# Kernel tuning notes

Hardware: AMD Instinct MI355X
Metric: run time of the kernel (lower is better)

The kernel has to match this reference:

```python
import jax, jax.numpy as jnp
import numpy as np

N, M, F0, FB, F, H, NC, NCONV = 60000, 12, 92, 41, 64, 128, 2000, 3
EPS = 1e-5


def setup_inputs() -> dict:
    key = jax.random.key(0)
    ks = jax.random.split(key, 12)
    s = 0.05
    return {
        "atom_fea": jax.random.normal(ks[0], (N, F0), jnp.float32),
        "nbr_fea": jax.random.normal(ks[1], (N, M, FB), jnp.float32),
        "nbr_fea_idx": jax.random.randint(ks[2], (N, M), 0, N),
        "crystal_atom_idx": jnp.sort(jax.random.randint(ks[3], (N,), 0, NC)),
        "W_emb": jax.random.normal(ks[4], (F0, F), jnp.float32) * s,
        "b_emb": jnp.zeros((F,), jnp.float32),
        "W_full": jax.random.normal(ks[5], (NCONV, 2 * F + FB, 2 * F), jnp.float32) * s,
        "b_full": jnp.zeros((NCONV, 2 * F), jnp.float32),
        "g1": jnp.ones((NCONV, 2 * F), jnp.float32),
        "be1": jnp.zeros((NCONV, 2 * F), jnp.float32),
        "g2": jnp.ones((NCONV, F), jnp.float32),
        "be2": jnp.zeros((NCONV, F), jnp.float32),
        "W_fc": jax.random.normal(ks[6], (F, H), jnp.float32) * s,
        "b_fc": jnp.zeros((H,), jnp.float32),
        "W_out": jax.random.normal(ks[7], (H, 1), jnp.float32) * s,
        "b_out": jnp.zeros((1,), jnp.float32),
    }


def _bn(x, g, b):
    # training-mode batch norm over leading (row) dim
    m = x.mean(axis=0)
    v = x.var(axis=0)
    return (x - m) * jax.lax.rsqrt(v + EPS) * g + b


def _conv_layer(x, nbr_fea, nbr_fea_idx, Wf, bf, g1, be1, g2, be2):
    n, m = nbr_fea_idx.shape
    f = x.shape[1]
    atom_nbr = x[nbr_fea_idx]  # (N, M, F) gather
    total = jnp.concatenate(
        [jnp.broadcast_to(x[:, None, :], (n, m, f)), atom_nbr, nbr_fea], axis=2
    )  # (N, M, 2F+FB)
    gated = total @ Wf + bf  # (N, M, 2F)
    gated = _bn(gated.reshape(-1, 2 * f), g1, be1).reshape(n, m, 2 * f)
    nbr_filter, nbr_core = jnp.split(gated, 2, axis=2)
    summed = jnp.sum(jax.nn.sigmoid(nbr_filter) * jax.nn.softplus(nbr_core), axis=1)
    summed = _bn(summed, g2, be2)
    return jax.nn.softplus(x + summed)


def reference(atom_fea, nbr_fea, nbr_fea_idx, crystal_atom_idx, W_emb, b_emb,
              W_full, b_full, g1, be1, g2, be2, W_fc, b_fc, W_out, b_out):
    x = atom_fea @ W_emb + b_emb  # (N, F)
    for i in range(NCONV):
        x = _conv_layer(x, nbr_fea, nbr_fea_idx, W_full[i], b_full[i],
                        g1[i], be1[i], g2[i], be2[i])
    # mean-pool atoms per crystal (segment mean)
    sums = jax.ops.segment_sum(x, crystal_atom_idx, num_segments=NC)
    cnt = jax.ops.segment_sum(jnp.ones((x.shape[0],), x.dtype), crystal_atom_idx,
                              num_segments=NC)
    crys = sums / jnp.maximum(cnt, 1.0)[:, None]  # (NC, F)
    crys = jax.nn.softplus(crys) @ W_fc + b_fc
    crys = jax.nn.softplus(crys)
    return crys @ W_out + b_out  # (NC, 1)
```

## Files before the change

kernel.cpp:

```cpp
#include <hip/hip_runtime.h>
#include <hip/hip_bf16.h>


#define NATOM 60000
#define MNBR  12
#define F0D   92
#define FBD   41
#define FD    64
#define F2D   128
#define NCRY  2000
#define HD    128
#define NSUP  15000
#define GS    132

#define OFF_X      0ull
#define OFF_XH     3840000ull
#define OFF_SUMMED 5760000ull
#define OFF_STATS  9600000ull
#define OFF_CRYS   9600384ull
#define OFF_CNT    9728384ull
#define OFF_WCONV  9730384ull
#define OFF_WBF    9811220ull
#define OFF_FLAG   9848084ull
#define WS_NEED_BYTES (9848085ull * 4ull)

#define W_EMB_O  0
#define B_EMB_O  5888
#define W_FULL_O 5952
#define B_FULL_O 70848
#define G1_O     71232
#define BE1_O    71616
#define G2_O     72000
#define BE2_O    72192
#define W_FC_O   72384
#define B_FC_O   80576
#define W_OUT_O  80704
#define B_OUT_O  80832
#define WC_TOTAL 80833

typedef unsigned short u16;
typedef __attribute__((ext_vector_type(8))) short bf16x8;
typedef __attribute__((ext_vector_type(4))) float f32x4;

__device__ __forceinline__ float bf2f(u16 u){
  union { unsigned int i; float f; } v; v.i = ((unsigned int)u) << 16; return v.f;
}
__device__ __forceinline__ u16 f2bf(float f){
  union { float f; unsigned int i; } v; v.f = f;
  unsigned int x = v.i;
  return (u16)((x + 0x7FFFu + ((x >> 16) & 1u)) >> 16);
}
__device__ __forceinline__ float softplusf_(float x){
  return fmaxf(x, 0.f) + log1pf(expf(-fabsf(x)));
}
__device__ __forceinline__ float softplus_fast(float x){
  return fmaxf(x, 0.f) + __logf(1.f + __expf(-fabsf(x)));
}
__device__ __forceinline__ float sigmoid_fast(float x){
  return __builtin_amdgcn_rcpf(1.f + __expf(-x));
}

__global__ __launch_bounds__(64) void detect_kernel(
    const u16* __restrict__ data, int* __restrict__ flag){
  int tid = threadIdx.x;
  float v = bf2f(data[tid * 2]);
  float av = fabsf(v);
  bool sane = (av > 1e-6f) && (av < 100.f);
  unsigned long long m = __ballot(sane);
  if (tid == 0) *flag = (__popcll(m) >= 32) ? 1 : 0;
}

struct CvtArgs {
  const void* src[12];
  int start[13];
};

__global__ __launch_bounds__(256) void cvt_all_kernel(
    CvtArgs a, float* __restrict__ dst, const int* __restrict__ flag){
  int i = blockIdx.x * 256 + threadIdx.x;
  if (i >= WC_TOTAL) return;
  int r = 0;
  while (i >= a.start[r + 1]) r++;
  int rel = i - a.start[r];
  if (*flag) dst[i] = bf2f(((const u16*)a.src[r])[rel]);
  else       dst[i] = ((const float*)a.src[r])[rel];
}

__global__ __launch_bounds__(256) void build_bfrag(
    const float* __restrict__ wfull, u16* __restrict__ wbf){
  int t = blockIdx.x * 256 + threadIdx.x;
  if (t >= 3 * 6 * 8 * 64) return;
  int lane = t & 63, nt = (t >> 6) & 7, c = (t >> 9) % 6, layer = t / 3072;
  int q = lane >> 4, nloc = lane & 15;
  u16 vals[8];
  #pragma unroll
  for (int i = 0; i < 8; i++){
    int k = c * 32 + q * 8 + i;
    float v = (k < 169) ? wfull[layer * 169 * F2D + k * F2D + nt * 16 + nloc] : 0.f;
    vals[i] = f2bf(v);
  }
  *(uint4*)&wbf[(size_t)t * 8] = *(uint4*)vals;
}

__global__ __launch_bounds__(256) void embed_kernel(
    const void* __restrict__ atom_fea, const float* __restrict__ W_emb,
    const float* __restrict__ b_emb, float* __restrict__ x,
    u16* __restrict__ xh, const int* __restrict__ flag){
  int tid = threadIdx.x;
  int n = blockIdx.x * 4 + (tid >> 6);
  int f = tid & 63;
  float acc = b_emb[f];
  if (*flag){
    const u16* arow = (const u16*)atom_fea + n * F0D;
    for (int k = 0; k < F0D; k++)
      acc = fmaf(bf2f(arow[k]), W_emb[k * FD + f], acc);
  } else {
    const float* arow = (const float*)atom_fea + n * F0D;
    for (int k = 0; k < F0D; k++)
      acc = fmaf(arow[k], W_emb[k * FD + f], acc);
  }
  x[n * FD + f] = acc;
  xh[n * FD + f] = f2bf(acc);
}

template<int ACT>
__global__ __launch_bounds__(256, 3) void conv_mfma(
    const u16* __restrict__ xh, const void* __restrict__ nbr_fea,
    const int* __restrict__ nbr_idx, const u16* __restrict__ wbf_l,
    const float* __restrict__ bfull, const float* __restrict__ sum1,
    const float* __restrict__ sq1, const float* __restrict__ g1,
    const float* __restrict__ be1, float* __restrict__ summed,
    float* __restrict__ o_sum, float* __restrict__ o_sq,
    const int* __restrict__ flag){
  extern __shared__ char smem[];
  u16*   fragA = (u16*)smem;
  float* gbuf  = (float*)(smem + 6144);
  float* redS  = ACT ? (gbuf + 48 * GS) : (float*)(smem + 6144);
  float* redQ  = redS + (ACT ? 64 : 128);

  const int tid = threadIdx.x;
  const int w = tid >> 6, lane = tid & 63;
  const int q = lane >> 4, nloc = lane & 15, q8 = q * 8;
  const int isbf = *flag;

  bf16x8 Bf[6][2];
  const bf16x8* Bv = (const bf16x8*)wbf_l;
  #pragma unroll
  for (int c = 0; c < 6; c++)
    #pragma unroll
    for (int t2 = 0; t2 < 2; t2++)
      Bf[c][t2] = Bv[(c * 8 + w * 2 + t2) * 64 + lane];
  float bias0 = bfull[w * 32 + nloc];
  float bias1 = bfull[w * 32 + 16 + nloc];

  float A0 = 0.f, B0 = 0.f, A1 = 0.f, B1 = 0.f;
  if (ACT){
    const float invR = 1.f / (float)(NATOM * MNBR);
    float m0 = sum1[lane] * invR;
    float v0 = fmaxf(sq1[lane] * invR - m0 * m0, 0.f);
    A0 = g1[lane] * rsqrtf(v0 + 1e-5f);  B0 = be1[lane] - m0 * A0;
    float m1 = sum1[64 + lane] * invR;
    float v1 = fmaxf(sq1[64 + lane] * invR - m1 * m1, 0.f);
    A1 = g1[64 + lane] * rsqrtf(v1 + 1e-5f);  B1 = be1[64 + lane] - m1 * A1;
  }
  float sAcc0 = 0.f, sAcc1 = 0.f, qAcc0 = 0.f, qAcc1 = 0.f;
  if (tid < (ACT ? 64 : 128)){ redS[tid] = 0.f; redQ[tid] = 0.f; }

  const bf16x8* xv = (const bf16x8*)xh;
  for (int s = blockIdx.x; s < NSUP; s += gridDim.x){
    if (w < 3){
      size_t eg = (size_t)(s * 48 + w * 16 + nloc);
      u16 v4[8], v5[8];
      if (isbf){
        const u16* br = (const u16*)nbr_fea + eg * 41;
        #pragma unroll
        for (int i = 0; i < 8; i++) v4[i] = br[q8 + i];
        #pragma unroll
        for (int i = 0; i < 8; i++){
          int k5 = 32 + q8 + i;
          v5[i] = (k5 < 41) ? br[(k5 < 41) ? k5 : 0] : (u16)0;
        }
      } else {
        const float* br = (const float*)nbr_fea + eg * 41;
        #pragma unroll
        for (int i = 0; i < 8; i++) v4[i] = f2bf(br[q8 + i]);
        #pragma unroll
        for (int i = 0; i < 8; i++){
          int k5 = 32 + q8 + i;
          v5[i] = (k5 < 41) ? f2bf(br[(k5 < 41) ? k5 : 0]) : (u16)0;
        }
      }
      *(uint4*)&fragA[(w * 2 + 0) * 512 + lane * 8] = *(uint4*)v4;
      *(uint4*)&fragA[(w * 2 + 1) * 512 + lane * 8] = *(uint4*)v5;
    }
    int e0 = s * 48 + nloc;
    int nb0 = nbr_idx[e0], nb1 = nbr_idx[e0 + 16], nb2 = nbr_idx[e0 + 32];
    __syncthreads();
    #pragma unroll
    for (int et = 0; et < 3; et++){
      int nb = (et == 0) ? nb0 : (et == 1) ? nb1 : nb2;
      int na = s * 4 + (et * 16 + nloc) / 12;
      bf16x8 a0 = xv[na * 8 + q];
      bf16x8 a1 = xv[na * 8 + 4 + q];
      bf16x8 a2 = xv[nb * 8 + q];
      bf16x8 a3 = xv[nb * 8 + 4 + q];
      bf16x8 a4 = *(bf16x8*)&fragA[(et * 2 + 0) * 512 + lane * 8];
      bf16x8 a5 = *(bf16x8*)&fragA[(et * 2 + 1) * 512 + lane * 8];
      #pragma unroll
      for (int t2 = 0; t2 < 2; t2++){
        float bs = t2 ? bias1 : bias0;
        f32x4 acc = {bs, bs, bs, bs};
        acc = __builtin_amdgcn_mfma_f32_16x16x32_bf16(a0, Bf[0][t2], acc, 0, 0, 0);
        acc = __builtin_amdgcn_mfma_f32_16x16x32_bf16(a1, Bf[1][t2], acc, 0, 0, 0);
        acc = __builtin_amdgcn_mfma_f32_16x16x32_bf16(a2, Bf[2][t2], acc, 0, 0, 0);
        acc = __builtin_amdgcn_mfma_f32_16x16x32_bf16(a3, Bf[3][t2], acc, 0, 0, 0);
        acc = __builtin_amdgcn_mfma_f32_16x16x32_bf16(a4, Bf[4][t2], acc, 0, 0, 0);
        acc = __builtin_amdgcn_mfma_f32_16x16x32_bf16(a5, Bf[5][t2], acc, 0, 0, 0);
        if (ACT){
          int col = w * 32 + t2 * 16 + nloc;
          int r0 = et * 16 + q * 4;
          gbuf[(r0 + 0) * GS + col] = acc[0];
          gbuf[(r0 + 1) * GS + col] = acc[1];
          gbuf[(r0 + 2) * GS + col] = acc[2];
          gbuf[(r0 + 3) * GS + col] = acc[3];
        } else {
          float ss = acc[0] + acc[1] + acc[2] + acc[3];
          float qq = acc[0]*acc[0] + acc[1]*acc[1] + acc[2]*acc[2] + acc[3]*acc[3];
          if (t2){ sAcc1 += ss; qAcc1 += qq; } else { sAcc0 += ss; qAcc0 += qq; }
        }
      }
    }
    if (ACT){
      __syncthreads();
      float p = 0.f;
      #pragma unroll
      for (int m = 0; m < 12; m++){
        int el = w * 12 + m;
        float u = fmaf(gbuf[el * GS + lane],      A0, B0);
        float v = fmaf(gbuf[el * GS + 64 + lane], A1, B1);
        p = fmaf(sigmoid_fast(u), softplus_fast(v), p);
      }
      summed[(s * 4 + w) * 64 + lane] = p;
      sAcc0 += p;  qAcc0 = fmaf(p, p, qAcc0);
    }
    __syncthreads();
  }
  if (ACT){
    atomicAdd(&redS[lane], sAcc0);
    atomicAdd(&redQ[lane], qAcc0);
    __syncthreads();
    if (tid < 64){ atomicAdd(&o_sum[tid], redS[tid]); atomicAdd(&o_sq[tid], redQ[tid]); }
  } else {
    int c0 = w * 32 + nloc;
    atomicAdd(&redS[c0], sAcc0);       atomicAdd(&redQ[c0], qAcc0);
    atomicAdd(&redS[c0 + 16], sAcc1);  atomicAdd(&redQ[c0 + 16], qAcc1);
    __syncthreads();
    if (tid < 128){ atomicAdd(&o_sum[tid], redS[tid]); atomicAdd(&o_sq[tid], redQ[tid]); }
  }
}

__global__ __launch_bounds__(256) void update_x_kernel(
    float* __restrict__ x, u16* __restrict__ xh,
    const float* __restrict__ summed,
    const float* __restrict__ sum2, const float* __restrict__ sq2,
    const float* __restrict__ g2, const float* __restrict__ be2){
  int idx = blockIdx.x * 256 + threadIdx.x;
  int f = idx & 63;
  const float invN = 1.f / (float)NATOM;
  float mean = sum2[f] * invN;
  float var  = fmaxf(sq2[f] * invN - mean * mean, 0.f);
  float a = g2[f] * rsqrtf(var + 1e-5f);
  float b = be2[f] - mean * a;
  float v = x[idx] + fmaf(summed[idx], a, b);
  float r = softplusf_(v);
  x[idx] = r;
  xh[idx] = f2bf(r);
}

__global__ __launch_bounds__(256) void pool_kernel(
    const float* __restrict__ x, const int* __restrict__ cidx,
    float* __restrict__ crys, float* __restrict__ cnt){
  int idx = blockIdx.x * 256 + threadIdx.x;
  int n = idx >> 6, f = idx & 63;
  int c = cidx[n];
  atomicAdd(&crys[c * FD + f], x[idx]);
  if (f == 0) atomicAdd(&cnt[c], 1.f);
}

__global__ __launch_bounds__(128) void head_kernel(
    const float* __restrict__ crys, const float* __restrict__ cnt,
    const float* __restrict__ W_fc, const float* __restrict__ b_fc,
    const float* __restrict__ W_out, const float* __restrict__ b_out,
    void* __restrict__ out, const int* __restrict__ flag){
  __shared__ float p_s[FD];
  __shared__ float red_s[HD];
  int c = blockIdx.x, tid = threadIdx.x;
  if (tid < FD){
    float ct = fmaxf(cnt[c], 1.f);
    p_s[tid] = softplusf_(crys[c * FD + tid] / ct);
  }
  __syncthreads();
  float acc = b_fc[tid];
  for (int k = 0; k < FD; k++)
    acc = fmaf(p_s[k], W_fc[k * HD + tid], acc);
  float h = softplusf_(acc);
  red_s[tid] = h * W_out[tid];
  __syncthreads();
  for (int s = HD / 2; s > 0; s >>= 1){
    if (tid < s) red_s[tid] += red_s[tid + s];
    __syncthreads();
  }
  if (tid == 0){
    float r = red_s[0] + b_out[0];
    if (*flag) ((u16*)out)[c] = f2bf(r);
    else       ((float*)out)[c] = r;
  }
}

extern "C" void kernel_launch(void* const* d_in, const int* in_sizes, int n_in,
                              void* d_out, int out_size, void* d_ws, size_t ws_size,
                              hipStream_t stream){
  if (ws_size < WS_NEED_BYTES) return;
  const void* atom_fea = d_in[0];
  const void* nbr_fea  = d_in[1];
  const int* nbr_idx   = (const int*)d_in[2];
  const int* cidx      = (const int*)d_in[3];

  float* ws     = (float*)d_ws;
  float* x      = ws + OFF_X;
  u16*   xh     = (u16*)(ws + OFF_XH);
  float* summed = ws + OFF_SUMMED;
  float* sum1   = ws + OFF_STATS;
  float* sq1    = sum1 + 128;
  float* sum2   = sq1 + 128;
  float* sq2    = sum2 + 64;
  float* crys   = ws + OFF_CRYS;
  float* cnt    = ws + OFF_CNT;
  float* wc     = ws + OFF_WCONV;
  u16*   wbf    = (u16*)(ws + OFF_WBF);
  int*   flag   = (int*)(ws + OFF_FLAG);

  detect_kernel<<<1, 64, 0, stream>>>((const u16*)nbr_fea, flag);
  CvtArgs ca;
  const int srcidx[12] = {4,5,6,7,8,9,10,11,12,13,14,15};
  const int starts[13] = {W_EMB_O, B_EMB_O, W_FULL_O, B_FULL_O, G1_O, BE1_O,
                          G2_O, BE2_O, W_FC_O, B_FC_O, W_OUT_O, B_OUT_O, WC_TOTAL};
  for (int i = 0; i < 12; i++){ ca.src[i] = d_in[srcidx[i]]; ca.start[i] = starts[i]; }
  ca.start[12] = WC_TOTAL;
  cvt_all_kernel<<<(WC_TOTAL + 255) / 256, 256, 0, stream>>>(ca, wc, flag);
  build_bfrag<<<(9216 + 255) / 256, 256, 0, stream>>>(wc + W_FULL_O, wbf);

  embed_kernel<<<NATOM / 4, 256, 0, stream>>>(atom_fea, wc + W_EMB_O, wc + B_EMB_O,
                                              x, xh, flag);
  const int LDS_STATS = 6144 + 2 * 128 * 4;
  const int LDS_ACT   = 6144 + (48 * GS + 128) * 4;
  for (int i = 0; i < 3; i++){
    const u16* wbf_l = wbf + (size_t)i * 3072 * 8;
    hipMemsetAsync(sum1, 0, 384 * sizeof(float), stream);
    conv_mfma<0><<<3000, 256, LDS_STATS, stream>>>(xh, nbr_fea, nbr_idx, wbf_l,
        wc + B_FULL_O + i * F2D, sum1, sq1, wc + G1_O + i * F2D,
        wc + BE1_O + i * F2D, summed, sum1, sq1, flag);
    conv_mfma<1><<<3000, 256, LDS_ACT, stream>>>(xh, nbr_fea, nbr_idx, wbf_l,
        wc + B_FULL_O + i * F2D, sum1, sq1, wc + G1_O + i * F2D,
        wc + BE1_O + i * F2D, summed, sum2, sq2, flag);
    update_x_kernel<<<(NATOM * FD) / 256, 256, 0, stream>>>(x, xh, summed, sum2, sq2,
        wc + G2_O + i * FD, wc + BE2_O + i * FD);
  }
  hipMemsetAsync(crys, 0, (NCRY * FD + NCRY) * sizeof(float), stream);
  pool_kernel<<<(NATOM * FD) / 256, 256, 0, stream>>>(x, cidx, crys, cnt);
  head_kernel<<<NCRY, 128, 0, stream>>>(crys, cnt, wc + W_FC_O, wc + B_FC_O,
      wc + W_OUT_O, wc + B_OUT_O, d_out, flag);
}
```

Measured before the change: 1.100 ms.

## Pre-pad bond features into bf16 MFMA-ready layout once, load fragments directly

Adds a bond_prep kernel that converts nbr_fea once into a padded bf16 array with 48 elements per edge. Both conv passes in all three layers then load MFMA A fragments straight from global memory instead of staging them through LDS, which removes the per-iteration fragment build and a __syncthreads in the stats pass. The cost is an extra pass over nbr_fea and about 69 MB of workspace. The old path is kept as a fallback when the workspace is too small, so the new path only runs if the harness provides enough workspace.

```diff
diff --git a/kernel.cpp b/kernel.cpp
--- a/kernel.cpp
+++ b/kernel.cpp
@@ -23,6 +23,8 @@
 #define OFF_WBF    9811220ull
 #define OFF_FLAG   9848084ull
 #define WS_NEED_BYTES (9848085ull * 4ull)
+#define OFF_BPAD   9848088ull
+#define WS_FULL_BYTES ((OFF_BPAD + 17280000ull) * 4ull)
 
 #define W_EMB_O  0
 #define B_EMB_O  5888
@@ -100,6 +102,35 @@
     vals[i] = f2bf(v);
   }
   *(uint4*)&wbf[(size_t)t * 8] = *(uint4*)vals;
+}
+
+__global__ __launch_bounds__(256) void bond_prep(
+    const void* __restrict__ nbr_fea, u16* __restrict__ bond_pad,
+    const int* __restrict__ flag){
+  __shared__ __align__(16) char sm[7872];
+  u16*   lb_u = (u16*)sm;
+  float* lb_f = (float*)sm;
+  int s = blockIdx.x, tid = threadIdx.x;
+  const int isbf = *flag;
+  if (isbf){
+    const uint4* src = (const uint4*)((const u16*)nbr_fea + (size_t)s * 1968);
+    if (tid < 246) ((uint4*)sm)[tid] = src[tid];
+  } else {
+    const uint4* src = (const uint4*)((const float*)nbr_fea + (size_t)s * 1968);
+    for (int t = tid; t < 492; t += 256) ((uint4*)sm)[t] = src[t];
+  }
+  __syncthreads();
+  uint4* outv = (uint4*)(bond_pad + (size_t)s * 2304);
+  for (int slot = tid; slot < 288; slot += 256){
+    int el = slot / 6, jj = slot - el * 6;
+    u16 v[8];
+    #pragma unroll
+    for (int i = 0; i < 8; i++){
+      int k = jj * 8 + i;
+      v[i] = (k < FBD) ? (isbf ? lb_u[el * FBD + k] : f2bf(lb_f[el * FBD + k])) : (u16)0;
+    }
+    outv[slot] = *(uint4*)v;
+  }
 }
 
 __global__ __launch_bounds__(256) void embed_kernel(
@@ -123,9 +154,10 @@
   xh[n * FD + f] = f2bf(acc);
 }
 
-template<int ACT>
+template<int ACT, int PAD>
 __global__ __launch_bounds__(256, 3) void conv_mfma(
     const u16* __restrict__ xh, const void* __restrict__ nbr_fea,
+    const u16* __restrict__ bond_pad,
     const int* __restrict__ nbr_idx, const u16* __restrict__ wbf_l,
     const float* __restrict__ bfull, const float* __restrict__ sum1,
     const float* __restrict__ sq1, const float* __restrict__ g1,
@@ -134,8 +166,9 @@
     const int* __restrict__ flag){
   extern __shared__ char smem[];
   u16*   fragA = (u16*)smem;
-  float* gbuf  = (float*)(smem + 6144);
-  float* redS  = ACT ? (gbuf + 48 * GS) : (float*)(smem + 6144);
+  const int base_off = PAD ? 0 : 6144;
+  float* gbuf  = (float*)(smem + base_off);
+  float* redS  = ACT ? (gbuf + 48 * GS) : (float*)(smem + base_off);
   float* redQ  = redS + (ACT ? 64 : 128);
 
   const int tid = threadIdx.x;
@@ -165,57 +198,78 @@
   }
   float sAcc0 = 0.f, sAcc1 = 0.f, qAcc0 = 0.f, qAcc1 = 0.f;
   if (tid < (ACT ? 64 : 128)){ redS[tid] = 0.f; redQ[tid] = 0.f; }
+  if (PAD && !ACT) ;
 
   const bf16x8* xv = (const bf16x8*)xh;
+  const bf16x8 zero8 = {0,0,0,0,0,0,0,0};
   for (int s = blockIdx.x; s < NSUP; s += gridDim.x){
-    if (w < 3){
-      size_t eg = (size_t)(s * 48 + w * 16 + nloc);
-      u16 v4[8], v5[8];
-      if (isbf){
-        const u16* br = (const u16*)nbr_fea + eg * 41;
-        #pragma unroll
-        for (int i = 0; i < 8; i++) v4[i] = br[q8 + i];
-        #pragma unroll
-        for (int i = 0; i < 8; i++){
-          int k5 = 32 + q8 + i;
-          v5[i] = (k5 < 41) ? br[(k5 < 41) ? k5 : 0] : (u16)0;
-        }
-      } else {
-        const float* br = (const float*)nbr_fea + eg * 41;
-        #pragma unroll
-        for (int i = 0; i < 8; i++) v4[i] = f2bf(br[q8 + i]);
-        #pragma unroll
-        for (int i = 0; i < 8; i++){
-          int k5 = 32 + q8 + i;
-          v5[i] = (k5 < 41) ? f2bf(br[(k5 < 41) ? k5 : 0]) : (u16)0;
-        }
-      }
-      *(uint4*)&fragA[(w * 2 + 0) * 512 + lane * 8] = *(uint4*)v4;
-      *(uint4*)&fragA[(w * 2 + 1) * 512 + lane * 8] = *(uint4*)v5;
-    }
     int e0 = s * 48 + nloc;
     int nb0 = nbr_idx[e0], nb1 = nbr_idx[e0 + 16], nb2 = nbr_idx[e0 + 32];
-    __syncthreads();
+    bf16x8 Af[3][6];
+    if (PAD){
+      #pragma unroll
+      for (int et = 0; et < 3; et++){
+        int nb = (et == 0) ? nb0 : (et == 1) ? nb1 : nb2;
+        int na = s * 4 + (et * 16 + nloc) / 12;
+        Af[et][0] = xv[na * 8 + q];
+        Af[et][1] = xv[na * 8 + 4 + q];
+        Af[et][2] = xv[nb * 8 + q];
+        Af[et][3] = xv[nb * 8 + 4 + q];
+        const bf16x8* bpv = (const bf16x8*)(bond_pad + (size_t)(e0 + et * 16) * 48);
+        Af[et][4] = bpv[q];
+        Af[et][5] = (q < 2) ? bpv[4 + q] : zero8;
+      }
+    } else {
+      if (w < 3){
+        size_t eg = (size_t)(s * 48 + w * 16 + nloc);
+        u16 v4[8], v5[8];
+        if (isbf){
+          const u16* br = (const u16*)nbr_fea + eg * 41;
+          #pragma unroll
+          for (int i = 0; i < 8; i++) v4[i] = br[q8 + i];
+          #pragma unroll
+          for (int i = 0; i < 8; i++){
+            int k5 = 32 + q8 + i;
+            v5[i] = (k5 < 41) ? br[k5] : (u16)0;
+          }
+        } else {
+          const float* br = (const float*)nbr_fea + eg * 41;
+          #pragma unroll
+          for (int i = 0; i < 8; i++) v4[i] = f2bf(br[q8 + i]);
+          #pragma unroll
+          for (int i = 0; i < 8; i++){
+            int k5 = 32 + q8 + i;
+            v5[i] = (k5 < 41) ? f2bf(br[k5]) : (u16)0;
+          }
+        }
+        *(uint4*)&fragA[(w * 2 + 0) * 512 + lane * 8] = *(uint4*)v4;
+        *(uint4*)&fragA[(w * 2 + 1) * 512 + lane * 8] = *(uint4*)v5;
+      }
+      __syncthreads();
+      #pragma unroll
+      for (int et = 0; et < 3; et++){
+        int nb = (et == 0) ? nb0 : (et == 1) ? nb1 : nb2;
+        int na = s * 4 + (et * 16 + nloc) / 12;
+        Af[et][0] = xv[na * 8 + q];
+        Af[et][1] = xv[na * 8 + 4 + q];
+        Af[et][2] = xv[nb * 8 + q];
+        Af[et][3] = xv[nb * 8 + 4 + q];
+        Af[et][4] = *(bf16x8*)&fragA[(et * 2 + 0) * 512 + lane * 8];
+        Af[et][5] = *(bf16x8*)&fragA[(et * 2 + 1) * 512 + lane * 8];
+      }
+    }
     #pragma unroll
     for (int et = 0; et < 3; et++){
-      int nb = (et == 0) ? nb0 : (et == 1) ? nb1 : nb2;
-      int na = s * 4 + (et * 16 + nloc) / 12;
-      bf16x8 a0 = xv[na * 8 + q];
-      bf16x8 a1 = xv[na * 8 + 4 + q];
-      bf16x8 a2 = xv[nb * 8 + q];
-      bf16x8 a3 = xv[nb * 8 + 4 + q];
-      bf16x8 a4 = *(bf16x8*)&fragA[(et * 2 + 0) * 512 + lane * 8];
-      bf16x8 a5 = *(bf16x8*)&fragA[(et * 2 + 1) * 512 + lane * 8];
       #pragma unroll
       for (int t2 = 0; t2 < 2; t2++){
         float bs = t2 ? bias1 : bias0;
         f32x4 acc = {bs, bs, bs, bs};
-        acc = __builtin_amdgcn_mfma_f32_16x16x32_bf16(a0, Bf[0][t2], acc, 0, 0, 0);
-        acc = __builtin_amdgcn_mfma_f32_16x16x32_bf16(a1, Bf[1][t2], acc, 0, 0, 0);
-        acc = __builtin_amdgcn_mfma_f32_16x16x32_bf16(a2, Bf[2][t2], acc, 0, 0, 0);
-        acc = __builtin_amdgcn_mfma_f32_16x16x32_bf16(a3, Bf[3][t2], acc, 0, 0, 0);
-        acc = __builtin_amdgcn_mfma_f32_16x16x32_bf16(a4, Bf[4][t2], acc, 0, 0, 0);
-        acc = __builtin_amdgcn_mfma_f32_16x16x32_bf16(a5, Bf[5][t2], acc, 0, 0, 0);
+        acc = __builtin_amdgcn_mfma_f32_16x16x32_bf16(Af[et][0], Bf[0][t2], acc, 0, 0, 0);
+        acc = __builtin_amdgcn_mfma_f32_16x16x32_bf16(Af[et][1], Bf[1][t2], acc, 0, 0, 0);
+        acc = __builtin_amdgcn_mfma_f32_16x16x32_bf16(Af[et][2], Bf[2][t2], acc, 0, 0, 0);
+        acc = __builtin_amdgcn_mfma_f32_16x16x32_bf16(Af[et][3], Bf[3][t2], acc, 0, 0, 0);
+        acc = __builtin_amdgcn_mfma_f32_16x16x32_bf16(Af[et][4], Bf[4][t2], acc, 0, 0, 0);
+        acc = __builtin_amdgcn_mfma_f32_16x16x32_bf16(Af[et][5], Bf[5][t2], acc, 0, 0, 0);
         if (ACT){
           int col = w * 32 + t2 * 16 + nloc;
           int r0 = et * 16 + q * 4;
@@ -242,9 +296,12 @@
       }
       summed[(s * 4 + w) * 64 + lane] = p;
       sAcc0 += p;  qAcc0 = fmaf(p, p, qAcc0);
+      __syncthreads();
+    } else if (!PAD){
+      __syncthreads();
     }
-    __syncthreads();
-  }
+  }
+  __syncthreads();
   if (ACT){
     atomicAdd(&redS[lane], sAcc0);
     atomicAdd(&redQ[lane], qAcc0);
@@ -321,6 +378,7 @@
                               void* d_out, int out_size, void* d_ws, size_t ws_size,
                               hipStream_t stream){
   if (ws_size < WS_NEED_BYTES) return;
+  const bool full = (ws_size >= WS_FULL_BYTES);
   const void* atom_fea = d_in[0];
   const void* nbr_fea  = d_in[1];
   const int* nbr_idx   = (const int*)d_in[2];
@@ -339,6 +397,7 @@
   float* wc     = ws + OFF_WCONV;
   u16*   wbf    = (u16*)(ws + OFF_WBF);
   int*   flag   = (int*)(ws + OFF_FLAG);
+  u16*   bpad   = (u16*)(ws + OFF_BPAD);
 
   detect_kernel<<<1, 64, 0, stream>>>((const u16*)nbr_fea, flag);
   CvtArgs ca;
@@ -349,20 +408,32 @@
   ca.start[12] = WC_TOTAL;
   cvt_all_kernel<<<(WC_TOTAL + 255) / 256, 256, 0, stream>>>(ca, wc, flag);
   build_bfrag<<<(9216 + 255) / 256, 256, 0, stream>>>(wc + W_FULL_O, wbf);
+  if (full) bond_prep<<<NSUP, 256, 0, stream>>>(nbr_fea, bpad, flag);
 
   embed_kernel<<<NATOM / 4, 256, 0, stream>>>(atom_fea, wc + W_EMB_O, wc + B_EMB_O,
                                               x, xh, flag);
-  const int LDS_STATS = 6144 + 2 * 128 * 4;
-  const int LDS_ACT   = 6144 + (48 * GS + 128) * 4;
+  const int LDS_STATS_P = 2 * 128 * 4;
+  const int LDS_ACT_P   = (48 * GS + 128) * 4;
+  const int LDS_STATS_F = 6144 + 2 * 128 * 4;
+  const int LDS_ACT_F   = 6144 + (48 * GS + 128) * 4;
   for (int i = 0; i < 3; i++){
     const u16* wbf_l = wbf + (size_t)i * 3072 * 8;
     hipMemsetAsync(sum1, 0, 384 * sizeof(float), stream);
-    conv_mfma<0><<<3000, 256, LDS_STATS, stream>>>(xh, nbr_fea, nbr_idx, wbf_l,
-        wc + B_FULL_O + i * F2D, sum1, sq1, wc + G1_O + i * F2D,
-        wc + BE1_O + i * F2D, summed, sum1, sq1, flag);
-    conv_mfma<1><<<3000, 256, LDS_ACT, stream>>>(xh, nbr_fea, nbr_idx, wbf_l,
-        wc + B_FULL_O + i * F2D, sum1, sq1, wc + G1_O + i * F2D,
-        wc + BE1_O + i * F2D, summed, sum2, sq2, flag);
+    if (full){
+      conv_mfma<0,1><<<3000, 256, LDS_STATS_P, stream>>>(xh, nbr_fea, bpad, nbr_idx,
+          wbf_l, wc + B_FULL_O + i * F2D, sum1, sq1, wc + G1_O + i * F2D,
+          wc + BE1_O + i * F2D, summed, sum1, sq1, flag);
+      conv_mfma<1,1><<<3000, 256, LDS_ACT_P, stream>>>(xh, nbr_fea, bpad, nbr_idx,
+          wbf_l, wc + B_FULL_O + i * F2D, sum1, sq1, wc + G1_O + i * F2D,
+          wc + BE1_O + i * F2D, summed, sum2, sq2, flag);
+    } else {
+      conv_mfma<0,0><<<3000, 256, LDS_STATS_F, stream>>>(xh, nbr_fea, bpad, nbr_idx,
+          wbf_l, wc + B_FULL_O + i * F2D, sum1, sq1, wc + G1_O + i * F2D,
+          wc + BE1_O + i * F2D, summed, sum1, sq1, flag);
+      conv_mfma<1,0><<<3000, 256, LDS_ACT_F, stream>>>(xh, nbr_fea, bpad, nbr_idx,
+          wbf_l, wc + B_FULL_O + i * F2D, sum1, sq1, wc + G1_O + i * F2D,
+          wc + BE1_O + i * F2D, summed, sum2, sq2, flag);
+    }
     update_x_kernel<<<(NATOM * FD) / 256, 256, 0, stream>>>(x, xh, summed, sum2, sq2,
         wc + G2_O + i * FD, wc + BE2_O + i * FD);
   }
```

Result: faster. 1.015 ms (-7.8%).
